# Performance work log

Hardware: AMD Instinct MI355X
Metric: run time of the kernel (lower is better)

Reference implementation:

```python
import jax, jax.numpy as jnp
import numpy as np

BETA = 0.25

def setup_inputs() -> dict:
    key = jax.random.key(0)
    k1, k2 = jax.random.split(key)
    x = jax.random.normal(k1, (16, 256, 32, 32), dtype=jnp.float32)
    emb_weight = jax.random.normal(k2, (8192, 256), dtype=jnp.float32) * 0.02
    return {"x": x, "emb_weight": emb_weight}

def reference(x, emb_weight):
    # b c h w -> b h w c
    xt = jnp.transpose(x, (0, 2, 3, 1))
    D = emb_weight.shape[1]
    xf = xt.reshape(-1, D)  # [N, D]
    # squared euclidean distances: [N, K]
    dist = (jnp.sum(xf * xf, axis=1, keepdims=True)
            + jnp.sum(emb_weight * emb_weight, axis=1)
            - 2.0 * xf @ emb_weight.T)
    indices = jnp.argmin(dist, axis=1)  # [N]
    x_q = emb_weight[indices].reshape(xt.shape)  # [B,H,W,D]
    sg = jax.lax.stop_gradient
    loss = (BETA * jnp.mean(jnp.square(sg(x_q) - xt))
            + jnp.mean(jnp.square(x_q - sg(xt))))
    # straight-through estimator
    x_q_st = xt + sg(x_q - xt)
    out = jnp.transpose(x_q_st, (0, 3, 1, 2))  # b h w c -> b c h w
    return out, loss, indices
```

## Files before the change

### kernel.cpp

```cpp
#include <hip/hip_runtime.h>

#define NPTS   16384
#define KCODES 8192
#define DDIM   256
#define HWSZ   1024
#define CHW    (DDIM * HWSZ)
#define OUT_ELEMS 4194304
#define LOSS_OFF  OUT_ELEMS
#define IDX_OFF   (OUT_ELEMS + 1)

#define PTB   64
#define CTILE 128
#define KC    64
#define NIT   256
#define XPITCH 264

typedef _Float16 half_t;
typedef __attribute__((ext_vector_type(8))) _Float16 half8;
typedef __attribute__((ext_vector_type(4))) float     v4f;

union HU { _Float16 h; unsigned short u; };

#define EHI_WORDS  (256 * 8192)
#define SE_OFF_B   (2 * EHI_WORDS * 2)

#define GLD16(gp, lp) __builtin_amdgcn_global_load_lds( \
    (const __attribute__((address_space(1))) unsigned int*)(gp), \
    (__attribute__((address_space(3))) unsigned int*)(lp), 16, 0, 0)

__global__ void prep_kernel(const float* __restrict__ emb,
                            unsigned short* __restrict__ ehi,
                            unsigned short* __restrict__ elo,
                            float* __restrict__ se)
{
    const int gw   = (blockIdx.x * 256 + threadIdx.x) >> 6;
    const int lane = threadIdx.x & 63;
    for (int i = 0; i < 8; ++i) {
        const int c = gw * 8 + i;
        const float4 v = *(const float4*)(emb + (size_t)c * DDIM + lane * 4);
        float ps = v.x * v.x;
        ps = fmaf(v.y, v.y, ps); ps = fmaf(v.z, v.z, ps); ps = fmaf(v.w, v.w, ps);
        float tot = ps;
        #pragma unroll
        for (int off = 1; off < 64; off <<= 1) tot += __shfl_xor(tot, off);
        if (lane == 0) se[c] = tot;
        const float E0 = v.x * 64.f, E1 = v.y * 64.f, E2 = v.z * 64.f, E3 = v.w * 64.f;
        const half_t h0 = (half_t)E0, h1 = (half_t)E1, h2 = (half_t)E2, h3 = (half_t)E3;
        const half_t l0 = (half_t)((E0 - (float)h0) * 2048.f);
        const half_t l1 = (half_t)((E1 - (float)h1) * 2048.f);
        const half_t l2 = (half_t)((E2 - (float)h2) * 2048.f);
        const half_t l3 = (half_t)((E3 - (float)h3) * 2048.f);
        HU a0, a1, a2, a3, b0, b1, b2, b3;
        a0.h = h0; a1.h = h1; a2.h = h2; a3.h = h3;
        b0.h = l0; b1.h = l1; b2.h = l2; b3.h = l3;
        const unsigned int uh0 = (unsigned)a0.u | ((unsigned)a1.u << 16);
        const unsigned int uh1 = (unsigned)a2.u | ((unsigned)a3.u << 16);
        const unsigned int ul0 = (unsigned)b0.u | ((unsigned)b1.u << 16);
        const unsigned int ul1 = (unsigned)b2.u | ((unsigned)b3.u << 16);
        const int ck = lane >> 4;
        const int kb = (lane & 15) >> 1;
        const int hf = lane & 1;
        const int T = c >> 7, r = c & 127;
        const size_t base = (((size_t)(T * 4 + ck) * 128 + r) * 64)
                          + (size_t)((kb ^ (r & 7)) * 8) + hf * 4;
        *(unsigned int*)&ehi[base]     = uh0;
        *(unsigned int*)&ehi[base + 2] = uh1;
        *(unsigned int*)&elo[base]     = ul0;
        *(unsigned int*)&elo[base + 2] = ul1;
    }
}

__launch_bounds__(512)
__global__ void vq_kernel(const float* __restrict__ x,
                          const unsigned short* __restrict__ ehi,
                          const unsigned short* __restrict__ elo,
                          const float* __restrict__ wse,
                          const float* __restrict__ emb,
                          float* __restrict__ out)
{
    __shared__ __align__(16) unsigned short ldsXH[PTB][XPITCH];
    __shared__ __align__(16) unsigned short ldsXL[PTB][XPITCH];
    __shared__ __align__(16) unsigned short ldsEH[2][8192];
    __shared__ __align__(16) unsigned short ldsEL[2][8192];
    __shared__ float  ldsRS[8][65];
    __shared__ float  ldsS[PTB];
    __shared__ float  ldsFD[8][32];
    __shared__ int    ldsFI[8][32];
    __shared__ int    ldsI[PTB];
    __shared__ double ldsL[8];

    const int t    = threadIdx.x;
    const int lane = t & 63;
    const int w    = t >> 6;
    const int n0   = blockIdx.x * PTB;
    const int b    = n0 / HWSZ;
    const int hw0  = n0 % HWSZ;
    const float* xs = x + (size_t)b * CHW + hw0;

    const int part = (w & 3) * 4096;
    #define STAGE(img, buf) do { \
        const char* _g = (const char*)((w < 4) ? ehi : elo) \
                       + (size_t)(img) * 16384 + part + lane * 16; \
        char* _l = (char*)((w < 4) ? ldsEH[buf] : ldsEL[buf]) + part; \
        GLD16(_g,          _l); \
        GLD16(_g + 1024,   _l + 1024); \
        GLD16(_g + 2048,   _l + 2048); \
        GLD16(_g + 3072,   _l + 3072); \
    } while (0)

    STAGE(0, 0);

    {
        const int p   = t & 63;
        const int seg = t >> 6;
        float a = 0.f;
        for (int i = 0; i < 32; ++i) {
            const int c = seg * 32 + i;
            const float v = xs[(size_t)c * HWSZ + p];
            const half_t hh = (half_t)v;
            const half_t hl = (half_t)((v - (float)hh) * 2048.0f);
            HU u0; u0.h = hh; ldsXH[p][c] = u0.u;
            HU u1; u1.h = hl; ldsXL[p][c] = u1.u;
            a = fmaf(v, v, a);
        }
        ldsRS[seg][p] = a;
    }
    __syncthreads();
    if (t < PTB) {
        float s = 0.f;
        for (int g = 0; g < 8; ++g) s += ldsRS[g][t];
        ldsS[t] = s;
    }
    __syncthreads();

    const int h32 = (w & 1) * 32;
    const int q32 = (w >> 1) * 32;
    const int ln  = lane & 15;
    const int qd  = lane >> 4;

    float s_frag[8];
    #pragma unroll
    for (int pbi = 0; pbi < 2; ++pbi)
        #pragma unroll
        for (int r = 0; r < 4; ++r)
            s_frag[pbi * 4 + r] = ldsS[h32 + pbi * 16 + qd * 4 + r];

    half8 aH[2][4][2], aL[2][4][2];
    #pragma unroll
    for (int pb = 0; pb < 2; ++pb)
        #pragma unroll
        for (int ck = 0; ck < 4; ++ck)
            #pragma unroll
            for (int kk = 0; kk < 2; ++kk) {
                const int ka = ck * KC + kk * 32 + qd * 8;
                aH[pb][ck][kk] = *(const half8*)&ldsXH[h32 + pb * 16 + ln][ka];
                aL[pb][ck][kk] = *(const half8*)&ldsXL[h32 + pb * 16 + ln][ka];
            }

    float best_d[8]; int best_i[8];
    #pragma unroll
    for (int i = 0; i < 8; ++i) { best_d[i] = 3.4e38f; best_i[i] = 0; }

    v4f acc_hh[2][2], acc_hl[2][2];
    float se0 = 0.f, se1 = 0.f;

    for (int tile = 0; tile < 64; ++tile) {
        #pragma unroll
        for (int i = 0; i < 2; ++i)
            #pragma unroll
            for (int j = 0; j < 2; ++j)
                #pragma unroll
                for (int r = 0; r < 4; ++r) { acc_hh[i][j][r] = 0.f; acc_hl[i][j][r] = 0.f; }
        #pragma unroll
        for (int ck = 0; ck < 4; ++ck) {
            const int it = tile * 4 + ck;
            __syncthreads();
            if (it + 1 < NIT) STAGE(it + 1, (ck + 1) & 1);
            if (ck == 2) {
                const int tb2 = tile * CTILE;
                se0 = wse[tb2 + q32 + ln];
                se1 = wse[tb2 + q32 + 16 + ln];
            }
            #pragma unroll
            for (int kk = 0; kk < 2; ++kk) {
                const int swz = ((kk * 4 + qd) ^ (ln & 7)) * 8;
                const int rL  = (q32 + ln) * 64;
                const int rH  = (q32 + 16 + ln) * 64;
                const half8 bh0 = *(const half8*)&ldsEH[ck & 1][rL + swz];
                const half8 bh1 = *(const half8*)&ldsEH[ck & 1][rH + swz];
                const half8 bl0 = *(const half8*)&ldsEL[ck & 1][rL + swz];
                const half8 bl1 = *(const half8*)&ldsEL[ck & 1][rH + swz];
                acc_hh[0][0] = __builtin_amdgcn_mfma_f32_16x16x32_f16(aH[0][ck][kk], bh0, acc_hh[0][0], 0, 0, 0);
                acc_hh[0][1] = __builtin_amdgcn_mfma_f32_16x16x32_f16(aH[0][ck][kk], bh1, acc_hh[0][1], 0, 0, 0);
                acc_hh[1][0] = __builtin_amdgcn_mfma_f32_16x16x32_f16(aH[1][ck][kk], bh0, acc_hh[1][0], 0, 0, 0);
                acc_hh[1][1] = __builtin_amdgcn_mfma_f32_16x16x32_f16(aH[1][ck][kk], bh1, acc_hh[1][1], 0, 0, 0);
                acc_hl[0][0] = __builtin_amdgcn_mfma_f32_16x16x32_f16(aH[0][ck][kk], bl0, acc_hl[0][0], 0, 0, 0);
                acc_hl[0][1] = __builtin_amdgcn_mfma_f32_16x16x32_f16(aH[0][ck][kk], bl1, acc_hl[0][1], 0, 0, 0);
                acc_hl[1][0] = __builtin_amdgcn_mfma_f32_16x16x32_f16(aH[1][ck][kk], bl0, acc_hl[1][0], 0, 0, 0);
                acc_hl[1][1] = __builtin_amdgcn_mfma_f32_16x16x32_f16(aH[1][ck][kk], bl1, acc_hl[1][1], 0, 0, 0);
                acc_hl[0][0] = __builtin_amdgcn_mfma_f32_16x16x32_f16(aL[0][ck][kk], bh0, acc_hl[0][0], 0, 0, 0);
                acc_hl[0][1] = __builtin_amdgcn_mfma_f32_16x16x32_f16(aL[0][ck][kk], bh1, acc_hl[0][1], 0, 0, 0);
                acc_hl[1][0] = __builtin_amdgcn_mfma_f32_16x16x32_f16(aL[1][ck][kk], bh0, acc_hl[1][0], 0, 0, 0);
                acc_hl[1][1] = __builtin_amdgcn_mfma_f32_16x16x32_f16(aL[1][ck][kk], bh1, acc_hl[1][1], 0, 0, 0);
            }
            if (ck == 3) {
                const int tb = tile * CTILE;
                #pragma unroll
                for (int csi = 0; csi < 2; ++csi) {
                    const float se   = csi ? se1 : se0;
                    const int   code = tb + q32 + csi * 16 + ln;
                    #pragma unroll
                    for (int pbi = 0; pbi < 2; ++pbi)
                        #pragma unroll
                        for (int r = 0; r < 4; ++r) {
                            const float m  = fmaf(acc_hl[pbi][csi][r], 4.8828125e-4f,
                                                  acc_hh[pbi][csi][r]) * 0.015625f;
                            const float T  = s_frag[pbi * 4 + r] + se;
                            const float dd = fmaf(-2.0f, m, T);
                            const int   s  = pbi * 4 + r;
                            if (dd < best_d[s]) { best_d[s] = dd; best_i[s] = code; }
                        }
                }
            }
        }
    }

    #pragma unroll
    for (int off = 1; off < 16; off <<= 1) {
        #pragma unroll
        for (int s = 0; s < 8; ++s) {
            const float d2 = __shfl_xor(best_d[s], off);
            const int   i2 = __shfl_xor(best_i[s], off);
            if (d2 < best_d[s] || (d2 == best_d[s] && i2 < best_i[s])) {
                best_d[s] = d2; best_i[s] = i2;
            }
        }
    }
    if (ln == 0) {
        #pragma unroll
        for (int pbi = 0; pbi < 2; ++pbi)
            #pragma unroll
            for (int r = 0; r < 4; ++r) {
                ldsFD[w][pbi * 16 + qd * 4 + r] = best_d[pbi * 4 + r];
                ldsFI[w][pbi * 16 + qd * 4 + r] = best_i[pbi * 4 + r];
            }
    }
    __syncthreads();
    if (t < PTB) {
        const int hh  = t >> 5;
        const int r32 = t & 31;
        float bd = 3.4e38f; int bi = 0;
        #pragma unroll
        for (int qq = 0; qq < 4; ++qq) {
            const int wv = hh + qq * 2;
            const float d2 = ldsFD[wv][r32];
            const int   i2 = ldsFI[wv][r32];
            if (d2 < bd || (d2 == bd && i2 < bi)) { bd = d2; bi = i2; }
        }
        ldsI[t] = bi;
        out[(size_t)IDX_OFF + n0 + t] = (float)bi;
    }
    __syncthreads();

    double lsum = 0.0;
    {
        const int p  = t & 63;
        const int cg = t >> 6;
        const int row = ldsI[p];
        const float* erow = emb + (size_t)row * DDIM;
        float* ob = out + (size_t)b * CHW + hw0 + p;
        for (int q = 0; q < 32; ++q) {
            const int c = cg * 32 + q;
            const float e  = erow[c];
            const float xx = xs[(size_t)c * HWSZ + p];
            const float diff = e - xx;
            ob[(size_t)c * HWSZ] = xx + diff;
            lsum += (double)diff * (double)diff;
        }
    }
    #pragma unroll
    for (int off = 32; off > 0; off >>= 1)
        lsum += __shfl_xor(lsum, off);
    if ((t & 63) == 0) ldsL[t >> 6] = lsum;
    __syncthreads();
    if (t == 0) {
        double tot = 0.0;
        #pragma unroll
        for (int wv = 0; wv < 8; ++wv) tot += ldsL[wv];
        atomicAdd(&out[LOSS_OFF], (float)(tot * (1.25 / 4194304.0)));
    }
}

extern "C" void kernel_launch(void* const* d_in, const int* in_sizes, int n_in,
                              void* d_out, int out_size, void* d_ws, size_t ws_size,
                              hipStream_t stream) {
    (void)in_sizes; (void)n_in; (void)out_size; (void)ws_size;
    const float* x   = (const float*)d_in[0];
    const float* emb = (const float*)d_in[1];
    float* out = (float*)d_out;
    unsigned short* ehi = (unsigned short*)d_ws;
    unsigned short* elo = ehi + EHI_WORDS;
    float*          wse = (float*)((char*)d_ws + SE_OFF_B);
    hipMemsetAsync((char*)d_out + (size_t)LOSS_OFF * sizeof(float), 0, sizeof(float), stream);
    prep_kernel<<<256, 256, 0, stream>>>(emb, ehi, elo, wse);
    vq_kernel<<<NPTS / PTB, 512, 0, stream>>>(x, ehi, elo, wse, emb, out);
}
```

Baseline: 275.4 us.

## Deepen codebook staging to four LDS buffers with half-tile barriers and setprio

```diff
diff --git a/kernel.cpp b/kernel.cpp
--- a/kernel.cpp
+++ b/kernel.cpp
@@ -14,6 +14,10 @@
 #define KC    64
 #define NIT   256
 #define XPITCH 264
+
+#define ARENA_B 133120
+#define XH_OFF  65536
+#define XL_OFF  99328
 
 typedef _Float16 half_t;
 typedef __attribute__((ext_vector_type(8))) _Float16 half8;
@@ -78,10 +82,7 @@
                           const float* __restrict__ emb,
                           float* __restrict__ out)
 {
-    __shared__ __align__(16) unsigned short ldsXH[PTB][XPITCH];
-    __shared__ __align__(16) unsigned short ldsXL[PTB][XPITCH];
-    __shared__ __align__(16) unsigned short ldsEH[2][8192];
-    __shared__ __align__(16) unsigned short ldsEL[2][8192];
+    __shared__ __align__(16) char ldsA[ARENA_B];
     __shared__ float  ldsRS[8][65];
     __shared__ float  ldsS[PTB];
     __shared__ float  ldsFD[8][32];
@@ -97,11 +98,14 @@
     const int hw0  = n0 % HWSZ;
     const float* xs = x + (size_t)b * CHW + hw0;
 
+    unsigned short* XHp = (unsigned short*)(ldsA + XH_OFF);
+    unsigned short* XLp = (unsigned short*)(ldsA + XL_OFF);
+
     const int part = (w & 3) * 4096;
-    #define STAGE(img, buf) do { \
+    #define STAGE(img, q) do { \
         const char* _g = (const char*)((w < 4) ? ehi : elo) \
                        + (size_t)(img) * 16384 + part + lane * 16; \
-        char* _l = (char*)((w < 4) ? ldsEH[buf] : ldsEL[buf]) + part; \
+        char* _l = ldsA + (size_t)(q) * 32768 + ((w < 4) ? 0 : 16384) + part; \
         GLD16(_g,          _l); \
         GLD16(_g + 1024,   _l + 1024); \
         GLD16(_g + 2048,   _l + 2048); \
@@ -109,6 +113,7 @@
     } while (0)
 
     STAGE(0, 0);
+    STAGE(1, 1);
 
     {
         const int p   = t & 63;
@@ -119,8 +124,8 @@
             const float v = xs[(size_t)c * HWSZ + p];
             const half_t hh = (half_t)v;
             const half_t hl = (half_t)((v - (float)hh) * 2048.0f);
-            HU u0; u0.h = hh; ldsXH[p][c] = u0.u;
-            HU u1; u1.h = hl; ldsXL[p][c] = u1.u;
+            HU u0; u0.h = hh; XHp[p * XPITCH + c] = u0.u;
+            HU u1; u1.h = hl; XLp[p * XPITCH + c] = u1.u;
             a = fmaf(v, v, a);
         }
         ldsRS[seg][p] = a;
@@ -153,9 +158,11 @@
             #pragma unroll
             for (int kk = 0; kk < 2; ++kk) {
                 const int ka = ck * KC + kk * 32 + qd * 8;
-                aH[pb][ck][kk] = *(const half8*)&ldsXH[h32 + pb * 16 + ln][ka];
-                aL[pb][ck][kk] = *(const half8*)&ldsXL[h32 + pb * 16 + ln][ka];
+                aH[pb][ck][kk] = *(const half8*)&XHp[(h32 + pb * 16 + ln) * XPITCH + ka];
+                aL[pb][ck][kk] = *(const half8*)&XLp[(h32 + pb * 16 + ln) * XPITCH + ka];
             }
+    asm volatile("s_waitcnt lgkmcnt(0)" ::: "memory");
+    __syncthreads();
 
     float best_d[8]; int best_i[8];
     #pragma unroll
@@ -164,63 +171,86 @@
     v4f acc_hh[2][2], acc_hl[2][2];
     float se0 = 0.f, se1 = 0.f;
 
+    const int rL = (q32 + ln) * 64;
+    const int rH = (q32 + 16 + ln) * 64;
+
+    #define CHUNK(CK) do { \
+        const unsigned short* EHp = (const unsigned short*)(ldsA + (CK) * 32768); \
+        const unsigned short* ELp = (const unsigned short*)(ldsA + (CK) * 32768 + 16384); \
+        _Pragma("unroll") \
+        for (int kk = 0; kk < 2; ++kk) { \
+            const int swz = ((kk * 4 + qd) ^ (ln & 7)) * 8; \
+            const half8 bh0 = *(const half8*)&EHp[rL + swz]; \
+            const half8 bh1 = *(const half8*)&EHp[rH + swz]; \
+            const half8 bl0 = *(const half8*)&ELp[rL + swz]; \
+            const half8 bl1 = *(const half8*)&ELp[rH + swz]; \
+            acc_hh[0][0] = __builtin_amdgcn_mfma_f32_16x16x32_f16(aH[0][CK][kk], bh0, acc_hh[0][0], 0, 0, 0); \
+            acc_hh[0][1] = __builtin_amdgcn_mfma_f32_16x16x32_f16(aH[0][CK][kk], bh1, acc_hh[0][1], 0, 0, 0); \
+            acc_hh[1][0] = __builtin_amdgcn_mfma_f32_16x16x32_f16(aH[1][CK][kk], bh0, acc_hh[1][0], 0, 0, 0); \
+            acc_hh[1][1] = __builtin_amdgcn_mfma_f32_16x16x32_f16(aH[1][CK][kk], bh1, acc_hh[1][1], 0, 0, 0); \
+            acc_hl[0][0] = __builtin_amdgcn_mfma_f32_16x16x32_f16(aH[0][CK][kk], bl0, acc_hl[0][0], 0, 0, 0); \
+            acc_hl[0][1] = __builtin_amdgcn_mfma_f32_16x16x32_f16(aH[0][CK][kk], bl1, acc_hl[0][1], 0, 0, 0); \
+            acc_hl[1][0] = __builtin_amdgcn_mfma_f32_16x16x32_f16(aH[1][CK][kk], bl0, acc_hl[1][0], 0, 0, 0); \
+            acc_hl[1][1] = __builtin_amdgcn_mfma_f32_16x16x32_f16(aH[1][CK][kk], bl1, acc_hl[1][1], 0, 0, 0); \
+            acc_hl[0][0] = __builtin_amdgcn_mfma_f32_16x16x32_f16(aL[0][CK][kk], bh0, acc_hl[0][0], 0, 0, 0); \
+            acc_hl[0][1] = __builtin_amdgcn_mfma_f32_16x16x32_f16(aL[0][CK][kk], bh1, acc_hl[0][1], 0, 0, 0); \
+            acc_hl[1][0] = __builtin_amdgcn_mfma_f32_16x16x32_f16(aL[1][CK][kk], bh0, acc_hl[1][0], 0, 0, 0); \
+            acc_hl[1][1] = __builtin_amdgcn_mfma_f32_16x16x32_f16(aL[1][CK][kk], bh1, acc_hl[1][1], 0, 0, 0); \
+        } \
+    } while (0)
+
     for (int tile = 0; tile < 64; ++tile) {
+        const int it0 = tile * 4;
+        __builtin_amdgcn_s_barrier();
+        STAGE(it0 + 2, 2);
+        STAGE(it0 + 3, 3);
+        asm volatile("s_waitcnt vmcnt(8)" ::: "memory");
+        __builtin_amdgcn_s_barrier();
+        __builtin_amdgcn_s_setprio(1);
         #pragma unroll
         for (int i = 0; i < 2; ++i)
             #pragma unroll
             for (int j = 0; j < 2; ++j)
                 #pragma unroll
                 for (int r = 0; r < 4; ++r) { acc_hh[i][j][r] = 0.f; acc_hl[i][j][r] = 0.f; }
-        #pragma unroll
-        for (int ck = 0; ck < 4; ++ck) {
-            const int it = tile * 4 + ck;
-            __syncthreads();
-            if (it + 1 < NIT) STAGE(it + 1, (ck + 1) & 1);
-            if (ck == 2) {
-                const int tb2 = tile * CTILE;
-                se0 = wse[tb2 + q32 + ln];
-                se1 = wse[tb2 + q32 + 16 + ln];
-            }
+        CHUNK(0);
+        CHUNK(1);
+        __builtin_amdgcn_s_setprio(0);
+        {
+            const int tb2 = tile * CTILE;
+            se0 = wse[tb2 + q32 + ln];
+            se1 = wse[tb2 + q32 + 16 + ln];
+        }
+        __builtin_amdgcn_s_barrier();
+        if (tile + 1 < 64) {
+            STAGE(it0 + 4, 0);
+            STAGE(it0 + 5, 1);
+            asm volatile("s_waitcnt vmcnt(8)" ::: "memory");
+        } else {
+            asm volatile("s_waitcnt vmcnt(0)" ::: "memory");
+        }
+        __builtin_amdgcn_s_barrier();
+        __builtin_amdgcn_s_setprio(1);
+        CHUNK(2);
+        CHUNK(3);
+        __builtin_amdgcn_s_setprio(0);
+        {
+            const int tb = tile * CTILE;
             #pragma unroll
-            for (int kk = 0; kk < 2; ++kk) {
-                const int swz = ((kk * 4 + qd) ^ (ln & 7)) * 8;
-                const int rL  = (q32 + ln) * 64;
-                const int rH  = (q32 + 16 + ln) * 64;
-                const half8 bh0 = *(const half8*)&ldsEH[ck & 1][rL + swz];
-                const half8 bh1 = *(const half8*)&ldsEH[ck & 1][rH + swz];
-                const half8 bl0 = *(const half8*)&ldsEL[ck & 1][rL + swz];
-                const half8 bl1 = *(const half8*)&ldsEL[ck & 1][rH + swz];
-                acc_hh[0][0] = __builtin_amdgcn_mfma_f32_16x16x32_f16(aH[0][ck][kk], bh0, acc_hh[0][0], 0, 0, 0);
-                acc_hh[0][1] = __builtin_amdgcn_mfma_f32_16x16x32_f16(aH[0][ck][kk], bh1, acc_hh[0][1], 0, 0, 0);
-                acc_hh[1][0] = __builtin_amdgcn_mfma_f32_16x16x32_f16(aH[1][ck][kk], bh0, acc_hh[1][0], 0, 0, 0);
-                acc_hh[1][1] = __builtin_amdgcn_mfma_f32_16x16x32_f16(aH[1][ck][kk], bh1, acc_hh[1][1], 0, 0, 0);
-                acc_hl[0][0] = __builtin_amdgcn_mfma_f32_16x16x32_f16(aH[0][ck][kk], bl0, acc_hl[0][0], 0, 0, 0);
-                acc_hl[0][1] = __builtin_amdgcn_mfma_f32_16x16x32_f16(aH[0][ck][kk], bl1, acc_hl[0][1], 0, 0, 0);
-                acc_hl[1][0] = __builtin_amdgcn_mfma_f32_16x16x32_f16(aH[1][ck][kk], bl0, acc_hl[1][0], 0, 0, 0);
-                acc_hl[1][1] = __builtin_amdgcn_mfma_f32_16x16x32_f16(aH[1][ck][kk], bl1, acc_hl[1][1], 0, 0, 0);
-                acc_hl[0][0] = __builtin_amdgcn_mfma_f32_16x16x32_f16(aL[0][ck][kk], bh0, acc_hl[0][0], 0, 0, 0);
-                acc_hl[0][1] = __builtin_amdgcn_mfma_f32_16x16x32_f16(aL[0][ck][kk], bh1, acc_hl[0][1], 0, 0, 0);
-                acc_hl[1][0] = __builtin_amdgcn_mfma_f32_16x16x32_f16(aL[1][ck][kk], bh0, acc_hl[1][0], 0, 0, 0);
-                acc_hl[1][1] = __builtin_amdgcn_mfma_f32_16x16x32_f16(aL[1][ck][kk], bh1, acc_hl[1][1], 0, 0, 0);
-            }
-            if (ck == 3) {
-                const int tb = tile * CTILE;
+            for (int csi = 0; csi < 2; ++csi) {
+                const float se   = csi ? se1 : se0;
+                const int   code = tb + q32 + csi * 16 + ln;
                 #pragma unroll
-                for (int csi = 0; csi < 2; ++csi) {
-                    const float se   = csi ? se1 : se0;
-                    const int   code = tb + q32 + csi * 16 + ln;
+                for (int pbi = 0; pbi < 2; ++pbi)
                     #pragma unroll
-                    for (int pbi = 0; pbi < 2; ++pbi)
-                        #pragma unroll
-                        for (int r = 0; r < 4; ++r) {
-                            const float m  = fmaf(acc_hl[pbi][csi][r], 4.8828125e-4f,
-                                                  acc_hh[pbi][csi][r]) * 0.015625f;
-                            const float T  = s_frag[pbi * 4 + r] + se;
-                            const float dd = fmaf(-2.0f, m, T);
-                            const int   s  = pbi * 4 + r;
-                            if (dd < best_d[s]) { best_d[s] = dd; best_i[s] = code; }
-                        }
-                }
+                    for (int r = 0; r < 4; ++r) {
+                        const float m  = fmaf(acc_hl[pbi][csi][r], 4.8828125e-4f,
+                                              acc_hh[pbi][csi][r]) * 0.015625f;
+                        const float T  = s_frag[pbi * 4 + r] + se;
+                        const float dd = fmaf(-2.0f, m, T);
+                        const int   s  = pbi * 4 + r;
+                        if (dd < best_d[s]) { best_d[s] = dd; best_i[s] = code; }
+                    }
             }
         }
     }
```

Measured after the change: 310.2 us. 1.13x slower.

## Load codebook fragments directly from global into registers, drop LDS staging

Applied to the files above, without the earlier changes.

```diff
diff --git a/kernel.cpp b/kernel.cpp
--- a/kernel.cpp
+++ b/kernel.cpp
@@ -11,8 +11,6 @@
 
 #define PTB   64
 #define CTILE 128
-#define KC    64
-#define NIT   256
 #define XPITCH 264
 
 typedef _Float16 half_t;
@@ -23,10 +21,6 @@
 
 #define EHI_WORDS  (256 * 8192)
 #define SE_OFF_B   (2 * EHI_WORDS * 2)
-
-#define GLD16(gp, lp) __builtin_amdgcn_global_load_lds( \
-    (const __attribute__((address_space(1))) unsigned int*)(gp), \
-    (__attribute__((address_space(3))) unsigned int*)(lp), 16, 0, 0)
 
 __global__ void prep_kernel(const float* __restrict__ emb,
                             unsigned short* __restrict__ ehi,
@@ -57,12 +51,7 @@
         const unsigned int uh1 = (unsigned)a2.u | ((unsigned)a3.u << 16);
         const unsigned int ul0 = (unsigned)b0.u | ((unsigned)b1.u << 16);
         const unsigned int ul1 = (unsigned)b2.u | ((unsigned)b3.u << 16);
-        const int ck = lane >> 4;
-        const int kb = (lane & 15) >> 1;
-        const int hf = lane & 1;
-        const int T = c >> 7, r = c & 127;
-        const size_t base = (((size_t)(T * 4 + ck) * 128 + r) * 64)
-                          + (size_t)((kb ^ (r & 7)) * 8) + hf * 4;
+        const size_t base = (size_t)c * DDIM + lane * 4;
         *(unsigned int*)&ehi[base]     = uh0;
         *(unsigned int*)&ehi[base + 2] = uh1;
         *(unsigned int*)&elo[base]     = ul0;
@@ -80,8 +69,6 @@
 {
     __shared__ __align__(16) unsigned short ldsXH[PTB][XPITCH];
     __shared__ __align__(16) unsigned short ldsXL[PTB][XPITCH];
-    __shared__ __align__(16) unsigned short ldsEH[2][8192];
-    __shared__ __align__(16) unsigned short ldsEL[2][8192];
     __shared__ float  ldsRS[8][65];
     __shared__ float  ldsS[PTB];
     __shared__ float  ldsFD[8][32];
@@ -96,19 +83,6 @@
     const int b    = n0 / HWSZ;
     const int hw0  = n0 % HWSZ;
     const float* xs = x + (size_t)b * CHW + hw0;
-
-    const int part = (w & 3) * 4096;
-    #define STAGE(img, buf) do { \
-        const char* _g = (const char*)((w < 4) ? ehi : elo) \
-                       + (size_t)(img) * 16384 + part + lane * 16; \
-        char* _l = (char*)((w < 4) ? ldsEH[buf] : ldsEL[buf]) + part; \
-        GLD16(_g,          _l); \
-        GLD16(_g + 1024,   _l + 1024); \
-        GLD16(_g + 2048,   _l + 2048); \
-        GLD16(_g + 3072,   _l + 3072); \
-    } while (0)
-
-    STAGE(0, 0);
 
     {
         const int p   = t & 63;
@@ -145,17 +119,21 @@
         for (int r = 0; r < 4; ++r)
             s_frag[pbi * 4 + r] = ldsS[h32 + pbi * 16 + qd * 4 + r];
 
-    half8 aH[2][4][2], aL[2][4][2];
+    half8 aH[2][4][2];
     #pragma unroll
     for (int pb = 0; pb < 2; ++pb)
         #pragma unroll
         for (int ck = 0; ck < 4; ++ck)
             #pragma unroll
-            for (int kk = 0; kk < 2; ++kk) {
-                const int ka = ck * KC + kk * 32 + qd * 8;
-                aH[pb][ck][kk] = *(const half8*)&ldsXH[h32 + pb * 16 + ln][ka];
-                aL[pb][ck][kk] = *(const half8*)&ldsXL[h32 + pb * 16 + ln][ka];
-            }
+            for (int kk = 0; kk < 2; ++kk)
+                aH[pb][ck][kk] = *(const half8*)&ldsXH[h32 + pb * 16 + ln][ck * 64 + kk * 32 + qd * 8];
+
+    const unsigned short* pHL = ehi + (size_t)(q32 + ln) * DDIM + qd * 8;
+    const unsigned short* pHH = ehi + (size_t)(q32 + 16 + ln) * DDIM + qd * 8;
+    const unsigned short* pLL = elo + (size_t)(q32 + ln) * DDIM + qd * 8;
+    const unsigned short* pLH = elo + (size_t)(q32 + 16 + ln) * DDIM + qd * 8;
+    const int xlL = (h32 + ln) * XPITCH + qd * 8;
+    const int xlH = (h32 + 16 + ln) * XPITCH + qd * 8;
 
     float best_d[8]; int best_i[8];
     #pragma unroll
@@ -164,63 +142,86 @@
     v4f acc_hh[2][2], acc_hl[2][2];
     float se0 = 0.f, se1 = 0.f;
 
+    half8 fA0, fA1, fA2, fA3, fA4, fA5, fA6, fA7;
+    half8 fB0, fB1, fB2, fB3, fB4, fB5, fB6, fB7;
+
+    #define PF(SET, TOFF, CKO) do { \
+        SET##0 = *(const half8*)(pHL + (TOFF) + (CKO)); \
+        SET##1 = *(const half8*)(pHH + (TOFF) + (CKO)); \
+        SET##2 = *(const half8*)(pLL + (TOFF) + (CKO)); \
+        SET##3 = *(const half8*)(pLH + (TOFF) + (CKO)); \
+        SET##4 = *(const half8*)(pHL + (TOFF) + (CKO) + 32); \
+        SET##5 = *(const half8*)(pHH + (TOFF) + (CKO) + 32); \
+        SET##6 = *(const half8*)(pLL + (TOFF) + (CKO) + 32); \
+        SET##7 = *(const half8*)(pLH + (TOFF) + (CKO) + 32); \
+    } while (0)
+
+    #define TRIPLE(A0, A1, L0, L1, BH0, BH1, BL0, BL1) do { \
+        acc_hh[0][0] = __builtin_amdgcn_mfma_f32_16x16x32_f16(A0, BH0, acc_hh[0][0], 0, 0, 0); \
+        acc_hh[0][1] = __builtin_amdgcn_mfma_f32_16x16x32_f16(A0, BH1, acc_hh[0][1], 0, 0, 0); \
+        acc_hh[1][0] = __builtin_amdgcn_mfma_f32_16x16x32_f16(A1, BH0, acc_hh[1][0], 0, 0, 0); \
+        acc_hh[1][1] = __builtin_amdgcn_mfma_f32_16x16x32_f16(A1, BH1, acc_hh[1][1], 0, 0, 0); \
+        acc_hl[0][0] = __builtin_amdgcn_mfma_f32_16x16x32_f16(A0, BL0, acc_hl[0][0], 0, 0, 0); \
+        acc_hl[0][1] = __builtin_amdgcn_mfma_f32_16x16x32_f16(A0, BL1, acc_hl[0][1], 0, 0, 0); \
+        acc_hl[1][0] = __builtin_amdgcn_mfma_f32_16x16x32_f16(A1, BL0, acc_hl[1][0], 0, 0, 0); \
+        acc_hl[1][1] = __builtin_amdgcn_mfma_f32_16x16x32_f16(A1, BL1, acc_hl[1][1], 0, 0, 0); \
+        acc_hl[0][0] = __builtin_amdgcn_mfma_f32_16x16x32_f16(L0, BH0, acc_hl[0][0], 0, 0, 0); \
+        acc_hl[0][1] = __builtin_amdgcn_mfma_f32_16x16x32_f16(L0, BH1, acc_hl[0][1], 0, 0, 0); \
+        acc_hl[1][0] = __builtin_amdgcn_mfma_f32_16x16x32_f16(L1, BH0, acc_hl[1][0], 0, 0, 0); \
+        acc_hl[1][1] = __builtin_amdgcn_mfma_f32_16x16x32_f16(L1, BH1, acc_hl[1][1], 0, 0, 0); \
+    } while (0)
+
+    #define DOCHUNK(SET, CK) do { \
+        { const half8 xl0 = *(const half8*)&ldsXL[0][xlL + (CK) * 64]; \
+          const half8 xl1 = *(const half8*)&ldsXL[0][xlH + (CK) * 64]; \
+          TRIPLE(aH[0][CK][0], aH[1][CK][0], xl0, xl1, SET##0, SET##1, SET##2, SET##3); } \
+        { const half8 xl0 = *(const half8*)&ldsXL[0][xlL + (CK) * 64 + 32]; \
+          const half8 xl1 = *(const half8*)&ldsXL[0][xlH + (CK) * 64 + 32]; \
+          TRIPLE(aH[0][CK][1], aH[1][CK][1], xl0, xl1, SET##4, SET##5, SET##6, SET##7); } \
+    } while (0)
+
+    PF(fA, 0, 0);
+
     for (int tile = 0; tile < 64; ++tile) {
+        const size_t toff = (size_t)tile * (CTILE * DDIM);
         #pragma unroll
         for (int i = 0; i < 2; ++i)
             #pragma unroll
             for (int j = 0; j < 2; ++j)
                 #pragma unroll
                 for (int r = 0; r < 4; ++r) { acc_hh[i][j][r] = 0.f; acc_hl[i][j][r] = 0.f; }
-        #pragma unroll
-        for (int ck = 0; ck < 4; ++ck) {
-            const int it = tile * 4 + ck;
-            __syncthreads();
-            if (it + 1 < NIT) STAGE(it + 1, (ck + 1) & 1);
-            if (ck == 2) {
-                const int tb2 = tile * CTILE;
-                se0 = wse[tb2 + q32 + ln];
-                se1 = wse[tb2 + q32 + 16 + ln];
-            }
+
+        PF(fB, toff, 64);
+        DOCHUNK(fA, 0);
+        PF(fA, toff, 128);
+        DOCHUNK(fB, 1);
+        PF(fB, toff, 192);
+        {
+            const int tb2 = tile * CTILE;
+            se0 = wse[tb2 + q32 + ln];
+            se1 = wse[tb2 + q32 + 16 + ln];
+        }
+        DOCHUNK(fA, 2);
+        if (tile != 63) PF(fA, toff + (size_t)(CTILE * DDIM), 0);
+        DOCHUNK(fB, 3);
+
+        {
+            const int tb = tile * CTILE;
             #pragma unroll
-            for (int kk = 0; kk < 2; ++kk) {
-                const int swz = ((kk * 4 + qd) ^ (ln & 7)) * 8;
-                const int rL  = (q32 + ln) * 64;
-                const int rH  = (q32 + 16 + ln) * 64;
-                const half8 bh0 = *(const half8*)&ldsEH[ck & 1][rL + swz];
-                const half8 bh1 = *(const half8*)&ldsEH[ck & 1][rH + swz];
-                const half8 bl0 = *(const half8*)&ldsEL[ck & 1][rL + swz];
-                const half8 bl1 = *(const half8*)&ldsEL[ck & 1][rH + swz];
-                acc_hh[0][0] = __builtin_amdgcn_mfma_f32_16x16x32_f16(aH[0][ck][kk], bh0, acc_hh[0][0], 0, 0, 0);
-                acc_hh[0][1] = __builtin_amdgcn_mfma_f32_16x16x32_f16(aH[0][ck][kk], bh1, acc_hh[0][1], 0, 0, 0);
-                acc_hh[1][0] = __builtin_amdgcn_mfma_f32_16x16x32_f16(aH[1][ck][kk], bh0, acc_hh[1][0], 0, 0, 0);
-                acc_hh[1][1] = __builtin_amdgcn_mfma_f32_16x16x32_f16(aH[1][ck][kk], bh1, acc_hh[1][1], 0, 0, 0);
-                acc_hl[0][0] = __builtin_amdgcn_mfma_f32_16x16x32_f16(aH[0][ck][kk], bl0, acc_hl[0][0], 0, 0, 0);
-                acc_hl[0][1] = __builtin_amdgcn_mfma_f32_16x16x32_f16(aH[0][ck][kk], bl1, acc_hl[0][1], 0, 0, 0);
-                acc_hl[1][0] = __builtin_amdgcn_mfma_f32_16x16x32_f16(aH[1][ck][kk], bl0, acc_hl[1][0], 0, 0, 0);
-                acc_hl[1][1] = __builtin_amdgcn_mfma_f32_16x16x32_f16(aH[1][ck][kk], bl1, acc_hl[1][1], 0, 0, 0);
-                acc_hl[0][0] = __builtin_amdgcn_mfma_f32_16x16x32_f16(aL[0][ck][kk], bh0, acc_hl[0][0], 0, 0, 0);
-                acc_hl[0][1] = __builtin_amdgcn_mfma_f32_16x16x32_f16(aL[0][ck][kk], bh1, acc_hl[0][1], 0, 0, 0);
-                acc_hl[1][0] = __builtin_amdgcn_mfma_f32_16x16x32_f16(aL[1][ck][kk], bh0, acc_hl[1][0], 0, 0, 0);
-                acc_hl[1][1] = __builtin_amdgcn_mfma_f32_16x16x32_f16(aL[1][ck][kk], bh1, acc_hl[1][1], 0, 0, 0);
-            }
-            if (ck == 3) {
-                const int tb = tile * CTILE;
+            for (int csi = 0; csi < 2; ++csi) {
+                const float se   = csi ? se1 : se0;
+                const int   code = tb + q32 + csi * 16 + ln;
                 #pragma unroll
-                for (int csi = 0; csi < 2; ++csi) {
-                    const float se   = csi ? se1 : se0;
-                    const int   code = tb + q32 + csi * 16 + ln;
+                for (int pbi = 0; pbi < 2; ++pbi)
                     #pragma unroll
-                    for (int pbi = 0; pbi < 2; ++pbi)
-                        #pragma unroll
-                        for (int r = 0; r < 4; ++r) {
-                            const float m  = fmaf(acc_hl[pbi][csi][r], 4.8828125e-4f,
-                                                  acc_hh[pbi][csi][r]) * 0.015625f;
-                            const float T  = s_frag[pbi * 4 + r] + se;
-                            const float dd = fmaf(-2.0f, m, T);
-                            const int   s  = pbi * 4 + r;
-                            if (dd < best_d[s]) { best_d[s] = dd; best_i[s] = code; }
-                        }
-                }
+                    for (int r = 0; r < 4; ++r) {
+                        const float m  = fmaf(acc_hl[pbi][csi][r], 4.8828125e-4f,
+                                              acc_hh[pbi][csi][r]) * 0.015625f;
+                        const float T  = s_frag[pbi * 4 + r] + se;
+                        const float dd = fmaf(-2.0f, m, T);
+                        const int   s  = pbi * 4 + r;
+                        if (dd < best_d[s]) { best_d[s] = dd; best_i[s] = code; }
+                    }
             }
         }
     }
```

Result: slower. 554.9 us (+101.5%).

## Double block to 1024 threads, each wave covering 16 codes per tile

Applied to the files above, without the earlier changes.

```diff
diff --git a/kernel.cpp b/kernel.cpp
--- a/kernel.cpp
+++ b/kernel.cpp
@@ -70,7 +70,7 @@
     }
 }
 
-__launch_bounds__(512)
+__launch_bounds__(1024)
 __global__ void vq_kernel(const float* __restrict__ x,
                           const unsigned short* __restrict__ ehi,
                           const unsigned short* __restrict__ elo,
@@ -82,12 +82,12 @@
     __shared__ __align__(16) unsigned short ldsXL[PTB][XPITCH];
     __shared__ __align__(16) unsigned short ldsEH[2][8192];
     __shared__ __align__(16) unsigned short ldsEL[2][8192];
-    __shared__ float  ldsRS[8][65];
+    __shared__ float  ldsRS[16][65];
     __shared__ float  ldsS[PTB];
-    __shared__ float  ldsFD[8][32];
-    __shared__ int    ldsFI[8][32];
+    __shared__ float  ldsFD[16][32];
+    __shared__ int    ldsFI[16][32];
     __shared__ int    ldsI[PTB];
-    __shared__ double ldsL[8];
+    __shared__ double ldsL[16];
 
     const int t    = threadIdx.x;
     const int lane = t & 63;
@@ -97,15 +97,13 @@
     const int hw0  = n0 % HWSZ;
     const float* xs = x + (size_t)b * CHW + hw0;
 
-    const int part = (w & 3) * 4096;
+    const int part = (w & 7) * 2048;
     #define STAGE(img, buf) do { \
-        const char* _g = (const char*)((w < 4) ? ehi : elo) \
+        const char* _g = (const char*)((w < 8) ? ehi : elo) \
                        + (size_t)(img) * 16384 + part + lane * 16; \
-        char* _l = (char*)((w < 4) ? ldsEH[buf] : ldsEL[buf]) + part; \
+        char* _l = (char*)((w < 8) ? ldsEH[buf] : ldsEL[buf]) + part; \
         GLD16(_g,          _l); \
         GLD16(_g + 1024,   _l + 1024); \
-        GLD16(_g + 2048,   _l + 2048); \
-        GLD16(_g + 3072,   _l + 3072); \
     } while (0)
 
     STAGE(0, 0);
@@ -114,8 +112,8 @@
         const int p   = t & 63;
         const int seg = t >> 6;
         float a = 0.f;
-        for (int i = 0; i < 32; ++i) {
-            const int c = seg * 32 + i;
+        for (int i = 0; i < 16; ++i) {
+            const int c = seg * 16 + i;
             const float v = xs[(size_t)c * HWSZ + p];
             const half_t hh = (half_t)v;
             const half_t hl = (half_t)((v - (float)hh) * 2048.0f);
@@ -128,13 +126,13 @@
     __syncthreads();
     if (t < PTB) {
         float s = 0.f;
-        for (int g = 0; g < 8; ++g) s += ldsRS[g][t];
+        for (int g = 0; g < 16; ++g) s += ldsRS[g][t];
         ldsS[t] = s;
     }
     __syncthreads();
 
     const int h32 = (w & 1) * 32;
-    const int q32 = (w >> 1) * 32;
+    const int q16 = (w >> 1) * 16;
     const int ln  = lane & 15;
     const int qd  = lane >> 4;
 
@@ -161,67 +159,49 @@
     #pragma unroll
     for (int i = 0; i < 8; ++i) { best_d[i] = 3.4e38f; best_i[i] = 0; }
 
-    v4f acc_hh[2][2], acc_hl[2][2];
-    float se0 = 0.f, se1 = 0.f;
+    v4f acc_hh[2], acc_hl[2];
+    float se0 = 0.f;
+
+    const int rr = (q16 + ln) * 64;
 
     for (int tile = 0; tile < 64; ++tile) {
         #pragma unroll
         for (int i = 0; i < 2; ++i)
             #pragma unroll
-            for (int j = 0; j < 2; ++j)
-                #pragma unroll
-                for (int r = 0; r < 4; ++r) { acc_hh[i][j][r] = 0.f; acc_hl[i][j][r] = 0.f; }
+            for (int r = 0; r < 4; ++r) { acc_hh[i][r] = 0.f; acc_hl[i][r] = 0.f; }
         #pragma unroll
         for (int ck = 0; ck < 4; ++ck) {
             const int it = tile * 4 + ck;
             __syncthreads();
             if (it + 1 < NIT) STAGE(it + 1, (ck + 1) & 1);
-            if (ck == 2) {
-                const int tb2 = tile * CTILE;
-                se0 = wse[tb2 + q32 + ln];
-                se1 = wse[tb2 + q32 + 16 + ln];
-            }
+            if (ck == 2)
+                se0 = wse[tile * CTILE + q16 + ln];
             #pragma unroll
             for (int kk = 0; kk < 2; ++kk) {
                 const int swz = ((kk * 4 + qd) ^ (ln & 7)) * 8;
-                const int rL  = (q32 + ln) * 64;
-                const int rH  = (q32 + 16 + ln) * 64;
-                const half8 bh0 = *(const half8*)&ldsEH[ck & 1][rL + swz];
-                const half8 bh1 = *(const half8*)&ldsEH[ck & 1][rH + swz];
-                const half8 bl0 = *(const half8*)&ldsEL[ck & 1][rL + swz];
-                const half8 bl1 = *(const half8*)&ldsEL[ck & 1][rH + swz];
-                acc_hh[0][0] = __builtin_amdgcn_mfma_f32_16x16x32_f16(aH[0][ck][kk], bh0, acc_hh[0][0], 0, 0, 0);
-                acc_hh[0][1] = __builtin_amdgcn_mfma_f32_16x16x32_f16(aH[0][ck][kk], bh1, acc_hh[0][1], 0, 0, 0);
-                acc_hh[1][0] = __builtin_amdgcn_mfma_f32_16x16x32_f16(aH[1][ck][kk], bh0, acc_hh[1][0], 0, 0, 0);
-                acc_hh[1][1] = __builtin_amdgcn_mfma_f32_16x16x32_f16(aH[1][ck][kk], bh1, acc_hh[1][1], 0, 0, 0);
-                acc_hl[0][0] = __builtin_amdgcn_mfma_f32_16x16x32_f16(aH[0][ck][kk], bl0, acc_hl[0][0], 0, 0, 0);
-                acc_hl[0][1] = __builtin_amdgcn_mfma_f32_16x16x32_f16(aH[0][ck][kk], bl1, acc_hl[0][1], 0, 0, 0);
-                acc_hl[1][0] = __builtin_amdgcn_mfma_f32_16x16x32_f16(aH[1][ck][kk], bl0, acc_hl[1][0], 0, 0, 0);
-                acc_hl[1][1] = __builtin_amdgcn_mfma_f32_16x16x32_f16(aH[1][ck][kk], bl1, acc_hl[1][1], 0, 0, 0);
-                acc_hl[0][0] = __builtin_amdgcn_mfma_f32_16x16x32_f16(aL[0][ck][kk], bh0, acc_hl[0][0], 0, 0, 0);
-                acc_hl[0][1] = __builtin_amdgcn_mfma_f32_16x16x32_f16(aL[0][ck][kk], bh1, acc_hl[0][1], 0, 0, 0);
-                acc_hl[1][0] = __builtin_amdgcn_mfma_f32_16x16x32_f16(aL[1][ck][kk], bh0, acc_hl[1][0], 0, 0, 0);
-                acc_hl[1][1] = __builtin_amdgcn_mfma_f32_16x16x32_f16(aL[1][ck][kk], bh1, acc_hl[1][1], 0, 0, 0);
-            }
-            if (ck == 3) {
-                const int tb = tile * CTILE;
+                const half8 bh = *(const half8*)&ldsEH[ck & 1][rr + swz];
+                const half8 bl = *(const half8*)&ldsEL[ck & 1][rr + swz];
+                acc_hh[0] = __builtin_amdgcn_mfma_f32_16x16x32_f16(aH[0][ck][kk], bh, acc_hh[0], 0, 0, 0);
+                acc_hh[1] = __builtin_amdgcn_mfma_f32_16x16x32_f16(aH[1][ck][kk], bh, acc_hh[1], 0, 0, 0);
+                acc_hl[0] = __builtin_amdgcn_mfma_f32_16x16x32_f16(aH[0][ck][kk], bl, acc_hl[0], 0, 0, 0);
+                acc_hl[1] = __builtin_amdgcn_mfma_f32_16x16x32_f16(aH[1][ck][kk], bl, acc_hl[1], 0, 0, 0);
+                acc_hl[0] = __builtin_amdgcn_mfma_f32_16x16x32_f16(aL[0][ck][kk], bh, acc_hl[0], 0, 0, 0);
+                acc_hl[1] = __builtin_amdgcn_mfma_f32_16x16x32_f16(aL[1][ck][kk], bh, acc_hl[1], 0, 0, 0);
+            }
+        }
+        {
+            const int code = tile * CTILE + q16 + ln;
+            #pragma unroll
+            for (int pbi = 0; pbi < 2; ++pbi)
                 #pragma unroll
-                for (int csi = 0; csi < 2; ++csi) {
-                    const float se   = csi ? se1 : se0;
-                    const int   code = tb + q32 + csi * 16 + ln;
-                    #pragma unroll
-                    for (int pbi = 0; pbi < 2; ++pbi)
-                        #pragma unroll
-                        for (int r = 0; r < 4; ++r) {
-                            const float m  = fmaf(acc_hl[pbi][csi][r], 4.8828125e-4f,
-                                                  acc_hh[pbi][csi][r]) * 0.015625f;
-                            const float T  = s_frag[pbi * 4 + r] + se;
-                            const float dd = fmaf(-2.0f, m, T);
-                            const int   s  = pbi * 4 + r;
-                            if (dd < best_d[s]) { best_d[s] = dd; best_i[s] = code; }
-                        }
+                for (int r = 0; r < 4; ++r) {
+                    const float m  = fmaf(acc_hl[pbi][r], 4.8828125e-4f,
+                                          acc_hh[pbi][r]) * 0.015625f;
+                    const float T  = s_frag[pbi * 4 + r] + se0;
+                    const float dd = fmaf(-2.0f, m, T);
+                    const int   s  = pbi * 4 + r;
+                    if (dd < best_d[s]) { best_d[s] = dd; best_i[s] = code; }
                 }
-            }
         }
     }
 
@@ -251,8 +231,8 @@
         const int r32 = t & 31;
         float bd = 3.4e38f; int bi = 0;
         #pragma unroll
-        for (int qq = 0; qq < 4; ++qq) {
-            const int wv = hh + qq * 2;
+        for (int g = 0; g < 8; ++g) {
+            const int wv = g * 2 + hh;
             const float d2 = ldsFD[wv][r32];
             const int   i2 = ldsFI[wv][r32];
             if (d2 < bd || (d2 == bd && i2 < bi)) { bd = d2; bi = i2; }
@@ -269,8 +249,8 @@
         const int row = ldsI[p];
         const float* erow = emb + (size_t)row * DDIM;
         float* ob = out + (size_t)b * CHW + hw0 + p;
-        for (int q = 0; q < 32; ++q) {
-            const int c = cg * 32 + q;
+        for (int q = 0; q < 16; ++q) {
+            const int c = cg * 16 + q;
             const float e  = erow[c];
             const float xx = xs[(size_t)c * HWSZ + p];
             const float diff = e - xx;
@@ -286,7 +266,7 @@
     if (t == 0) {
         double tot = 0.0;
         #pragma unroll
-        for (int wv = 0; wv < 8; ++wv) tot += ldsL[wv];
+        for (int wv = 0; wv < 16; ++wv) tot += ldsL[wv];
         atomicAdd(&out[LOSS_OFF], (float)(tot * (1.25 / 4194304.0)));
     }
 }
@@ -303,5 +283,5 @@
     float*          wse = (float*)((char*)d_ws + SE_OFF_B);
     hipMemsetAsync((char*)d_out + (size_t)LOSS_OFF * sizeof(float), 0, sizeof(float), stream);
     prep_kernel<<<256, 256, 0, stream>>>(emb, ehi, elo, wse);
-    vq_kernel<<<NPTS / PTB, 512, 0, stream>>>(x, ehi, elo, wse, emb, out);
+    vq_kernel<<<NPTS / PTB, 1024, 0, stream>>>(x, ehi, elo, wse, emb, out);
 }
```

Result: slower. 744.7 us (+170.4%).
